# Performance work log

Measured on AMD Instinct MI355X. Metric: run time of the kernel, lower is better.

## Reference

```python
import jax, jax.numpy as jnp
import numpy as np

TAU = 1.0
NORMALIZE = True
EPS = 1e-16


def setup_inputs() -> dict:
    key = jax.random.key(0)
    k1, k2 = jax.random.split(key)
    N, D = 8192, 512
    xi = jax.random.normal(k1, (N, D), dtype=jnp.float32)
    xj = jax.random.normal(k2, (N, D), dtype=jnp.float32)
    return {"xi": xi, "xj": xj}


def reference(xi, xj):
    # sim_mat: [N, N] pairwise similarities
    sim_mat = xi @ xj.T
    if NORMALIZE:
        ni = jnp.linalg.norm(xi, axis=1)  # [N]
        nj = jnp.linalg.norm(xj, axis=1)  # [N]
        sim_mat = sim_mat / jnp.clip(ni[:, None] * nj[None, :], EPS)
    sim_mat = jnp.exp(sim_mat / TAU)
    # matched-pair similarity (diagonal-like term), [N]
    if NORMALIZE:
        sim_match = jnp.exp(jnp.sum(xi * xj, axis=-1) / (ni * nj) / TAU)
    else:
        sim_match = jnp.exp(jnp.sum(xi * xj, axis=-1) / TAU)
    sim_match = jnp.concatenate([sim_match, sim_match], axis=0)  # [2N]
    norm_sum = jnp.exp(jnp.ones((xi.shape[0],), dtype=xi.dtype) / TAU)  # [N]
    row_sum = jnp.sum(sim_mat, axis=-1) - norm_sum  # [N]
    # the torch source divides a [2N] vector by [N]; intended NT-Xent tiles the
    # denominator over both symmetric halves (values identical either way)
    row_sum = jnp.concatenate([row_sum, row_sum], axis=0)  # [2N]
    loss = jnp.mean(-jnp.log(sim_match / row_sum))
    return loss
```

## Files before the change

kernel.cpp:

```cpp
#include <hip/hip_runtime.h>
#include <stdint.h>

#define NR 8192
#define DIM 512
#define BT 128
#define BK 64
#define NT (DIM / BK)

typedef unsigned short u16;
typedef __attribute__((ext_vector_type(8))) __bf16 bf16x8;
typedef __attribute__((ext_vector_type(4))) float f32x4;

static __device__ __forceinline__ u16 f2bf(float f) {
    union { float f; uint32_t u; } v; v.f = f;
    uint32_t u = v.u;
    u += 0x7FFFu + ((u >> 16) & 1u);
    return (u16)(u >> 16);
}

static __device__ __forceinline__ void gload_lds16(const void* g, void* l) {
    __builtin_amdgcn_global_load_lds(
        (__attribute__((address_space(1))) void*)(void*)g,
        (__attribute__((address_space(3))) void*)l,
        16, 0, 0);
}

__global__ void prep_kernel(const float* __restrict__ xi, const float* __restrict__ xj,
                            u16* __restrict__ xib, u16* __restrict__ xjb,
                            float* __restrict__ inv_ni, float* __restrict__ inv_nj,
                            float* __restrict__ diag, float* __restrict__ rowsum) {
    const int row = blockIdx.x;
    const int t = threadIdx.x;
    const float4 a = ((const float4*)(xi + (size_t)row * DIM))[t];
    const float4 b = ((const float4*)(xj + (size_t)row * DIM))[t];

    float ssi = a.x*a.x + a.y*a.y + a.z*a.z + a.w*a.w;
    float ssj = b.x*b.x + b.y*b.y + b.z*b.z + b.w*b.w;
    float dot = a.x*b.x + a.y*b.y + a.z*b.z + a.w*b.w;

    ushort4 av = { f2bf(a.x), f2bf(a.y), f2bf(a.z), f2bf(a.w) };
    ushort4 bv = { f2bf(b.x), f2bf(b.y), f2bf(b.z), f2bf(b.w) };
    ((ushort4*)(xib + (size_t)row * DIM))[t] = av;
    ((ushort4*)(xjb + (size_t)row * DIM))[t] = bv;

    #pragma unroll
    for (int m = 32; m >= 1; m >>= 1) {
        ssi += __shfl_xor(ssi, m, 64);
        ssj += __shfl_xor(ssj, m, 64);
        dot += __shfl_xor(dot, m, 64);
    }
    __shared__ float red[6];
    const int wave = t >> 6, lane = t & 63;
    if (lane == 0) { red[wave*3+0] = ssi; red[wave*3+1] = ssj; red[wave*3+2] = dot; }
    __syncthreads();
    if (t == 0) {
        float si = red[0] + red[3];
        float sj = red[1] + red[4];
        float d  = red[2] + red[5];
        float ini = rsqrtf(fmaxf(si, 1e-30f));
        float inj = rsqrtf(fmaxf(sj, 1e-30f));
        inv_ni[row] = ini;
        inv_nj[row] = inj;
        diag[row] = d * ini * inj;
        rowsum[row] = 0.0f;
    }
}

__global__ __launch_bounds__(256, 4)
void gemm_rowsum(const u16* __restrict__ A, const u16* __restrict__ B,
                 const float* __restrict__ inv_ni, const float* __restrict__ inv_nj,
                 float* __restrict__ rowsum) {
    __shared__ __align__(16) u16 ldsA[BT * BK];
    __shared__ __align__(16) u16 ldsB[BT * BK];

    const int tid = threadIdx.x;
    const int orig = blockIdx.x;
    const int xcd = orig & 7, kidx = orig >> 3;
    const int by = xcd * 8 + (kidx & 7);
    const int bx = kidx >> 3;
    const int row0 = by * BT, col0 = bx * BT;

    const int st_row = tid >> 3;
    const int st_lc  = (tid & 7) ^ (st_row & 7);
    const u16* gA = A + (size_t)(row0 + st_row) * DIM + st_lc * 8;
    const u16* gB = B + (size_t)(col0 + st_row) * DIM + st_lc * 8;
    char* const dA = (char*)ldsA + tid * 16;
    char* const dB = (char*)ldsB + tid * 16;

    const int lane = tid & 63;
    const int lr = lane & 15, lk = lane >> 4;
    const int wid = tid >> 6;
    const int wm = wid >> 1, wn = wid & 1;
    const int sw = lr & 7;
    const int c0 = (lk ^ sw) * 16;
    const int c1 = ((4 + lk) ^ sw) * 16;
    const char* const aR = (const char*)ldsA + (wm * 64 + lr) * 128;
    const char* const bR = (const char*)ldsB + (wn * 64 + lr) * 128;

    f32x4 acc[4][4] = {};

    #pragma unroll 1
    for (int t = 0; t < NT; ++t) {
        if (t) __syncthreads();
        #pragma unroll
        for (int i = 0; i < 4; ++i) {
            gload_lds16(gA + t * BK + i * 32 * DIM, dA + i * 4096);
            gload_lds16(gB + t * BK + i * 32 * DIM, dB + i * 4096);
        }
        __syncthreads();

        #pragma unroll
        for (int kk = 0; kk < 2; ++kk) {
            const int cb = kk ? c1 : c0;
            bf16x8 af[4], bg[4];
            #pragma unroll
            for (int m = 0; m < 4; ++m)
                af[m] = *(const bf16x8*)(aR + m * 2048 + cb);
            #pragma unroll
            for (int n = 0; n < 4; ++n)
                bg[n] = *(const bf16x8*)(bR + n * 2048 + cb);
            #pragma unroll
            for (int m = 0; m < 4; ++m)
                #pragma unroll
                for (int n = 0; n < 4; ++n)
                    acc[m][n] = __builtin_amdgcn_mfma_f32_16x16x32_bf16(
                        af[m], bg[n], acc[m][n], 0, 0, 0);
        }
    }

    float inj[4];
    #pragma unroll
    for (int n = 0; n < 4; ++n)
        inj[n] = inv_nj[col0 + wn * 64 + n * 16 + lr];

    #pragma unroll
    for (int m = 0; m < 4; ++m) {
        #pragma unroll
        for (int e = 0; e < 4; ++e) {
            const int row = row0 + wm * 64 + m * 16 + lk * 4 + e;
            const float in_i = inv_ni[row];
            float s = 0.0f;
            #pragma unroll
            for (int n = 0; n < 4; ++n)
                s += __expf(acc[m][n][e] * in_i * inj[n]);
            s += __shfl_xor(s, 1, 64);
            s += __shfl_xor(s, 2, 64);
            s += __shfl_xor(s, 4, 64);
            s += __shfl_xor(s, 8, 64);
            if (lr == 0)
                atomicAdd(&rowsum[row], s);
        }
    }
}

__global__ void finalize(const float* __restrict__ rowsum,
                         const float* __restrict__ diag,
                         float* __restrict__ out) {
    const float E1 = 2.7182818284590452f;
    float acc = 0.0f;
    for (int i = threadIdx.x; i < NR; i += 256)
        acc += __logf(rowsum[i] - E1) - diag[i];
    #pragma unroll
    for (int m = 32; m >= 1; m >>= 1)
        acc += __shfl_xor(acc, m, 64);
    __shared__ float red[4];
    const int wave = threadIdx.x >> 6, lane = threadIdx.x & 63;
    if (lane == 0) red[wave] = acc;
    __syncthreads();
    if (threadIdx.x == 0)
        out[0] = (red[0] + red[1] + red[2] + red[3]) * (1.0f / NR);
}

extern "C" void kernel_launch(void* const* d_in, const int* in_sizes, int n_in,
                              void* d_out, int out_size, void* d_ws, size_t ws_size,
                              hipStream_t stream) {
    const float* xi = (const float*)d_in[0];
    const float* xj = (const float*)d_in[1];

    char* ws = (char*)d_ws;
    u16* xib = (u16*)ws;
    u16* xjb = xib + (size_t)NR * DIM;
    float* inv_ni = (float*)(xjb + (size_t)NR * DIM);
    float* inv_nj = inv_ni + NR;
    float* diag   = inv_nj + NR;
    float* rowsum = diag + NR;

    prep_kernel<<<NR, 128, 0, stream>>>(xi, xj, xib, xjb, inv_ni, inv_nj, diag, rowsum);
    gemm_rowsum<<<(NR / BT) * (NR / BT), 256, 0, stream>>>(xib, xjb, inv_ni, inv_nj, rowsum);
    finalize<<<1, 256, 0, stream>>>(rowsum, diag, (float*)d_out);
}
```

Measured before the change: 113.5 us.

## Rewrite GEMM as 256x256 tile with 32x32 MFMA and double-buffered LDS pipeline

Grows the block tile to 256x256 with 16 waves. It switches to 32x32x16 bf16 MFMA and double-buffers the LDS stages so global-to-LDS loads for the next K tile overlap compute. LDS reads use inline asm with explicit lgkmcnt waits, sched barriers and setprio to interleave ds_reads with MFMAs. The goal is better data reuse per loaded byte and hiding load latency. The cost is 128KB of LDS per block, which caps occupancy, and a more fragile hand-scheduled, fully unrolled K loop.

```diff
diff --git a/kernel.cpp b/kernel.cpp
--- a/kernel.cpp
+++ b/kernel.cpp
@@ -3,13 +3,13 @@
 
 #define NR 8192
 #define DIM 512
-#define BT 128
+#define BT 256
 #define BK 64
 #define NT (DIM / BK)
 
 typedef unsigned short u16;
 typedef __attribute__((ext_vector_type(8))) __bf16 bf16x8;
-typedef __attribute__((ext_vector_type(4))) float f32x4;
+typedef __attribute__((ext_vector_type(16))) float f32x16;
 
 static __device__ __forceinline__ u16 f2bf(float f) {
     union { float f; uint32_t u; } v; v.f = f;
@@ -23,6 +23,10 @@
         (__attribute__((address_space(1))) void*)(void*)g,
         (__attribute__((address_space(3))) void*)l,
         16, 0, 0);
+}
+
+static __device__ __forceinline__ uint32_t lds_addr(const void* p) {
+    return (uint32_t)(uintptr_t)(__attribute__((address_space(3))) const void*)p;
 }
 
 __global__ void prep_kernel(const float* __restrict__ xi, const float* __restrict__ xj,
@@ -66,88 +70,123 @@
     }
 }
 
-__global__ __launch_bounds__(256, 4)
+__global__ __launch_bounds__(1024, 4)
 void gemm_rowsum(const u16* __restrict__ A, const u16* __restrict__ B,
                  const float* __restrict__ inv_ni, const float* __restrict__ inv_nj,
                  float* __restrict__ rowsum) {
-    __shared__ __align__(16) u16 ldsA[BT * BK];
-    __shared__ __align__(16) u16 ldsB[BT * BK];
+    __shared__ __align__(16) u16 lds[4][16384];
 
     const int tid = threadIdx.x;
     const int orig = blockIdx.x;
     const int xcd = orig & 7, kidx = orig >> 3;
-    const int by = xcd * 8 + (kidx & 7);
-    const int bx = kidx >> 3;
+    const int by = xcd * 4 + (kidx & 3);
+    const int bx = kidx >> 2;
     const int row0 = by * BT, col0 = bx * BT;
 
     const int st_row = tid >> 3;
     const int st_lc  = (tid & 7) ^ (st_row & 7);
     const u16* gA = A + (size_t)(row0 + st_row) * DIM + st_lc * 8;
     const u16* gB = B + (size_t)(col0 + st_row) * DIM + st_lc * 8;
-    char* const dA = (char*)ldsA + tid * 16;
-    char* const dB = (char*)ldsB + tid * 16;
+    char* const ldsb = (char*)&lds[0][0];
+    char* const dsta = ldsb + tid * 16;
+    char* const dstb = ldsb + 65536 + tid * 16;
 
     const int lane = tid & 63;
-    const int lr = lane & 15, lk = lane >> 4;
+    const int l31 = lane & 31, hh = lane >> 5, sw = lane & 7;
     const int wid = tid >> 6;
-    const int wm = wid >> 1, wn = wid & 1;
-    const int sw = lr & 7;
-    const int c0 = (lk ^ sw) * 16;
-    const int c1 = ((4 + lk) ^ sw) * 16;
-    const char* const aR = (const char*)ldsA + (wm * 64 + lr) * 128;
-    const char* const bR = (const char*)ldsB + (wn * 64 + lr) * 128;
-
-    f32x4 acc[4][4] = {};
-
-    #pragma unroll 1
-    for (int t = 0; t < NT; ++t) {
-        if (t) __syncthreads();
+    const int wm = wid >> 2, wn = wid & 3;
+    const uint32_t ldsA32 = lds_addr(ldsb);
+    const uint32_t aoff = (wm * 64 + l31) * 128;
+    const uint32_t boff = (wn * 64 + l31) * 128;
+    const uint32_t cof0 = (uint32_t)(((0*2 + hh) ^ sw) * 16);
+    const uint32_t cof1 = (uint32_t)(((1*2 + hh) ^ sw) * 16);
+    const uint32_t cof2 = (uint32_t)(((2*2 + hh) ^ sw) * 16);
+    const uint32_t cof3 = (uint32_t)(((3*2 + hh) ^ sw) * 16);
+
+    f32x16 acc[2][2] = {};
+    bf16x8 af0[2], bg0[2], af1[2], bg1[2];
+
+#define DSR(D, ADDR) asm volatile("ds_read_b128 %0, %1" : "=v"(D) : "v"(ADDR))
+#define LGKM(N) asm volatile("s_waitcnt lgkmcnt(" #N ")" ::: "memory")
+#define SB0() __builtin_amdgcn_sched_barrier(0)
+#define BARR() __builtin_amdgcn_s_barrier()
+
+#define STAGE(P, TN) do {                                                      \
+    gload_lds16(gA + (TN) * BK,             dsta + (P) * 32768);               \
+    gload_lds16(gA + (TN) * BK + 128 * DIM, dsta + (P) * 32768 + 16384);       \
+    gload_lds16(gB + (TN) * BK,             dstb + (P) * 32768);               \
+    gload_lds16(gB + (TN) * BK + 128 * DIM, dstb + (P) * 32768 + 16384);       \
+} while (0)
+
+#define MM(AF, BG) do {                                                        \
+    __builtin_amdgcn_s_setprio(1);                                             \
+    acc[0][0] = __builtin_amdgcn_mfma_f32_32x32x16_bf16(AF[0], BG[0], acc[0][0], 0, 0, 0); \
+    acc[0][1] = __builtin_amdgcn_mfma_f32_32x32x16_bf16(AF[0], BG[1], acc[0][1], 0, 0, 0); \
+    acc[1][0] = __builtin_amdgcn_mfma_f32_32x32x16_bf16(AF[1], BG[0], acc[1][0], 0, 0, 0); \
+    acc[1][1] = __builtin_amdgcn_mfma_f32_32x32x16_bf16(AF[1], BG[1], acc[1][1], 0, 0, 0); \
+    __builtin_amdgcn_s_setprio(0);                                             \
+} while (0)
+
+#define TILE(P, ST, TN, VMSTR) do {                                            \
+    if (ST) STAGE((P) ^ 1, (TN) + 1);                                          \
+    asm volatile("s_waitcnt vmcnt(" VMSTR ")" ::: "memory");                   \
+    BARR();                                                                    \
+    const uint32_t ab = ldsA32 + (P) * 32768 + aoff;                           \
+    const uint32_t bb = ldsA32 + 65536 + (P) * 32768 + boff;                   \
+    DSR(af0[0], ab + cof0); DSR(af0[1], ab + 4096 + cof0);                     \
+    DSR(bg0[0], bb + cof0); DSR(bg0[1], bb + 4096 + cof0);                     \
+    DSR(af1[0], ab + cof1); DSR(af1[1], ab + 4096 + cof1);                     \
+    DSR(bg1[0], bb + cof1); DSR(bg1[1], bb + 4096 + cof1);                     \
+    LGKM(4); SB0();                                                            \
+    MM(af0, bg0);                                                     \
+    DSR(af0[0], ab + cof2); DSR(af0[1], ab + 4096 + cof2);                     \
+    DSR(bg0[0], bb + cof2); DSR(bg0[1], bb + 4096 + cof2);                     \
+    LGKM(4); SB0();                                                            \
+    MM(af1, bg1);                                                     \
+    DSR(af1[0], ab + cof3); DSR(af1[1], ab + 4096 + cof3);                     \
+    DSR(bg1[0], bb + cof3); DSR(bg1[1], bb + 4096 + cof3);                     \
+    LGKM(4); SB0();                                                            \
+    MM(af0, bg0);                                                     \
+    LGKM(0); SB0();                                                            \
+    BARR();                                       \
+    MM(af1, bg1);                                         \
+} while (0)
+
+    STAGE(0, 0);
+    TILE(0, 1, 0, "4");
+    TILE(1, 1, 1, "4");
+    TILE(0, 1, 2, "4");
+    TILE(1, 1, 3, "4");
+    TILE(0, 1, 4, "4");
+    TILE(1, 1, 5, "4");
+    TILE(0, 1, 6, "4");
+    TILE(1, 0, 7, "0");
+
+#undef DSR
+#undef LGKM
+#undef SB0
+#undef BARR
+#undef STAGE
+#undef MM
+#undef TILE
+
+    const float inj0 = inv_nj[col0 + wn * 64 + l31];
+    const float inj1 = inv_nj[col0 + wn * 64 + 32 + l31];
+
+    #pragma unroll
+    for (int mi = 0; mi < 2; ++mi) {
         #pragma unroll
-        for (int i = 0; i < 4; ++i) {
-            gload_lds16(gA + t * BK + i * 32 * DIM, dA + i * 4096);
-            gload_lds16(gB + t * BK + i * 32 * DIM, dB + i * 4096);
-        }
-        __syncthreads();
-
-        #pragma unroll
-        for (int kk = 0; kk < 2; ++kk) {
-            const int cb = kk ? c1 : c0;
-            bf16x8 af[4], bg[4];
-            #pragma unroll
-            for (int m = 0; m < 4; ++m)
-                af[m] = *(const bf16x8*)(aR + m * 2048 + cb);
-            #pragma unroll
-            for (int n = 0; n < 4; ++n)
-                bg[n] = *(const bf16x8*)(bR + n * 2048 + cb);
-            #pragma unroll
-            for (int m = 0; m < 4; ++m)
-                #pragma unroll
-                for (int n = 0; n < 4; ++n)
-                    acc[m][n] = __builtin_amdgcn_mfma_f32_16x16x32_bf16(
-                        af[m], bg[n], acc[m][n], 0, 0, 0);
-        }
-    }
-
-    float inj[4];
-    #pragma unroll
-    for (int n = 0; n < 4; ++n)
-        inj[n] = inv_nj[col0 + wn * 64 + n * 16 + lr];
-
-    #pragma unroll
-    for (int m = 0; m < 4; ++m) {
-        #pragma unroll
-        for (int e = 0; e < 4; ++e) {
-            const int row = row0 + wm * 64 + m * 16 + lk * 4 + e;
-            const float in_i = inv_ni[row];
-            float s = 0.0f;
-            #pragma unroll
-            for (int n = 0; n < 4; ++n)
-                s += __expf(acc[m][n][e] * in_i * inj[n]);
+        for (int r = 0; r < 16; ++r) {
+            const int row = row0 + wm * 64 + mi * 32 + (r & 3) + 8 * (r >> 2) + 4 * hh;
+            const float ini = inv_ni[row];
+            float s = __expf(acc[mi][0][r] * ini * inj0)
+                    + __expf(acc[mi][1][r] * ini * inj1);
             s += __shfl_xor(s, 1, 64);
             s += __shfl_xor(s, 2, 64);
             s += __shfl_xor(s, 4, 64);
             s += __shfl_xor(s, 8, 64);
-            if (lr == 0)
+            s += __shfl_xor(s, 16, 64);
+            if (l31 == 0)
                 atomicAdd(&rowsum[row], s);
         }
     }
@@ -186,6 +225,6 @@
     float* rowsum = diag + NR;
 
     prep_kernel<<<NR, 128, 0, stream>>>(xi, xj, xib, xjb, inv_ni, inv_nj, diag, rowsum);
-    gemm_rowsum<<<(NR / BT) * (NR / BT), 256, 0, stream>>>(xib, xjb, inv_ni, inv_nj, rowsum);
+    gemm_rowsum<<<(NR / BT) * (NR / BT), 1024, 0, stream>>>(xib, xjb, inv_ni, inv_nj, rowsum);
     finalize<<<1, 256, 0, stream>>>(rowsum, diag, (float*)d_out);
 }
```

Result: slower. 192.5 us (+69.6%).

## Double-buffer A tile in LDS and load B fragments directly from global

Applied to the files above, without the earlier changes.

Double-buffers the A tile in LDS so the load of the next K-step overlaps the MFMA work on the current one, with a single barrier per iteration. The B operand is no longer staged through LDS; each wave reads its B fragments straight from global memory into registers. This removes LDS traffic and one barrier for B but adds uncoalesced global loads per wave that depend on L2 hits, and it lowers the occupancy hint to 3 blocks per CU.

```diff
diff --git a/kernel.cpp b/kernel.cpp
--- a/kernel.cpp
+++ b/kernel.cpp
@@ -66,12 +66,11 @@
     }
 }
 
-__global__ __launch_bounds__(256, 4)
+__global__ __launch_bounds__(256, 3)
 void gemm_rowsum(const u16* __restrict__ A, const u16* __restrict__ B,
                  const float* __restrict__ inv_ni, const float* __restrict__ inv_nj,
                  float* __restrict__ rowsum) {
-    __shared__ __align__(16) u16 ldsA[BT * BK];
-    __shared__ __align__(16) u16 ldsB[BT * BK];
+    __shared__ __align__(16) u16 ldsA[2][BT * BK];
 
     const int tid = threadIdx.x;
     const int orig = blockIdx.x;
@@ -83,50 +82,69 @@
     const int st_row = tid >> 3;
     const int st_lc  = (tid & 7) ^ (st_row & 7);
     const u16* gA = A + (size_t)(row0 + st_row) * DIM + st_lc * 8;
-    const u16* gB = B + (size_t)(col0 + st_row) * DIM + st_lc * 8;
     char* const dA = (char*)ldsA + tid * 16;
-    char* const dB = (char*)ldsB + tid * 16;
 
     const int lane = tid & 63;
-    const int lr = lane & 15, lk = lane >> 4;
+    const int lr = lane & 15, lk = lane >> 4, sw = lr & 7;
     const int wid = tid >> 6;
     const int wm = wid >> 1, wn = wid & 1;
-    const int sw = lr & 7;
-    const int c0 = (lk ^ sw) * 16;
-    const int c1 = ((4 + lk) ^ sw) * 16;
-    const char* const aR = (const char*)ldsA + (wm * 64 + lr) * 128;
-    const char* const bR = (const char*)ldsB + (wn * 64 + lr) * 128;
+    const char* const aR0 = (const char*)ldsA + (wm * 64 + lr) * 128;
+    const int cb0 = (lk ^ sw) * 16;
+    const int cb1 = ((4 + lk) ^ sw) * 16;
+    const u16* const gB = B + (size_t)(col0 + wn * 64 + lr) * DIM + lk * 8;
 
     f32x4 acc[4][4] = {};
+
+#define STAGE(P, TN) do {                                                      \
+    _Pragma("unroll") for (int i = 0; i < 4; ++i)                              \
+        gload_lds16(gA + (TN) * BK + i * 32 * DIM, dA + (P) * 16384 + i * 4096); \
+} while (0)
+
+    STAGE(0, 0);
+    asm volatile("s_waitcnt vmcnt(0)" ::: "memory");
+    __builtin_amdgcn_s_barrier();
 
     #pragma unroll 1
     for (int t = 0; t < NT; ++t) {
-        if (t) __syncthreads();
-        #pragma unroll
-        for (int i = 0; i < 4; ++i) {
-            gload_lds16(gA + t * BK + i * 32 * DIM, dA + i * 4096);
-            gload_lds16(gB + t * BK + i * 32 * DIM, dB + i * 4096);
-        }
-        __syncthreads();
-
-        #pragma unroll
-        for (int kk = 0; kk < 2; ++kk) {
-            const int cb = kk ? c1 : c0;
-            bf16x8 af[4], bg[4];
-            #pragma unroll
-            for (int m = 0; m < 4; ++m)
-                af[m] = *(const bf16x8*)(aR + m * 2048 + cb);
+        const int p = t & 1;
+        if (t < NT - 1) STAGE(p ^ 1, t + 1);
+
+        const u16* gBt = gB + t * BK;
+        const char* aR = aR0 + p * 16384;
+
+        bf16x8 bg[4], af[4];
+        #pragma unroll
+        for (int n = 0; n < 4; ++n)
+            bg[n] = *(const bf16x8*)(gBt + n * 16 * DIM);
+        #pragma unroll
+        for (int m = 0; m < 4; ++m)
+            af[m] = *(const bf16x8*)(aR + m * 2048 + cb0);
+        #pragma unroll
+        for (int m = 0; m < 4; ++m)
             #pragma unroll
             for (int n = 0; n < 4; ++n)
-                bg[n] = *(const bf16x8*)(bR + n * 2048 + cb);
+                acc[m][n] = __builtin_amdgcn_mfma_f32_16x16x32_bf16(
+                    af[m], bg[n], acc[m][n], 0, 0, 0);
+
+        #pragma unroll
+        for (int n = 0; n < 4; ++n)
+            bg[n] = *(const bf16x8*)(gBt + n * 16 * DIM + 32);
+        #pragma unroll
+        for (int m = 0; m < 4; ++m)
+            af[m] = *(const bf16x8*)(aR + m * 2048 + cb1);
+        #pragma unroll
+        for (int m = 0; m < 4; ++m)
             #pragma unroll
-            for (int m = 0; m < 4; ++m)
-                #pragma unroll
-                for (int n = 0; n < 4; ++n)
-                    acc[m][n] = __builtin_amdgcn_mfma_f32_16x16x32_bf16(
-                        af[m], bg[n], acc[m][n], 0, 0, 0);
+            for (int n = 0; n < 4; ++n)
+                acc[m][n] = __builtin_amdgcn_mfma_f32_16x16x32_bf16(
+                    af[m], bg[n], acc[m][n], 0, 0, 0);
+
+        if (t < NT - 1) {
+            asm volatile("s_waitcnt vmcnt(0)" ::: "memory");
+            __builtin_amdgcn_s_barrier();
         }
     }
+#undef STAGE
 
     float inj[4];
     #pragma unroll
@@ -138,11 +156,11 @@
         #pragma unroll
         for (int e = 0; e < 4; ++e) {
             const int row = row0 + wm * 64 + m * 16 + lk * 4 + e;
-            const float in_i = inv_ni[row];
+            const float ini = inv_ni[row];
             float s = 0.0f;
             #pragma unroll
             for (int n = 0; n < 4; ++n)
-                s += __expf(acc[m][n][e] * in_i * inj[n]);
+                s += __expf(acc[m][n][e] * ini * inj[n]);
             s += __shfl_xor(s, 1, 64);
             s += __shfl_xor(s, 2, 64);
             s += __shfl_xor(s, 4, 64);
```

Measured after the change: 176.1 us. 1.55x slower.

## Double-buffer LDS tiles with BK=32 to overlap global loads with MFMA

Applied to the files above, without the earlier changes.

Halves the K tile to 32 and adds two LDS buffers, so the next tile's global-to-LDS loads are issued before computing on the current one. A single barrier per iteration replaces the two barriers around load and compute. The LDS swizzle is reworked for the 64-byte row stride. The trade-off is twice as many loop iterations and barriers, and only 16 MFMAs per barrier instead of 32.

```diff
diff --git a/kernel.cpp b/kernel.cpp
--- a/kernel.cpp
+++ b/kernel.cpp
@@ -4,7 +4,7 @@
 #define NR 8192
 #define DIM 512
 #define BT 128
-#define BK 64
+#define BK 32
 #define NT (DIM / BK)
 
 typedef unsigned short u16;
@@ -70,8 +70,8 @@
 void gemm_rowsum(const u16* __restrict__ A, const u16* __restrict__ B,
                  const float* __restrict__ inv_ni, const float* __restrict__ inv_nj,
                  float* __restrict__ rowsum) {
-    __shared__ __align__(16) u16 ldsA[BT * BK];
-    __shared__ __align__(16) u16 ldsB[BT * BK];
+    __shared__ __align__(16) u16 ldsA[2][BT * BK];
+    __shared__ __align__(16) u16 ldsB[2][BT * BK];
 
     const int tid = threadIdx.x;
     const int orig = blockIdx.x;
@@ -80,8 +80,8 @@
     const int bx = kidx >> 3;
     const int row0 = by * BT, col0 = bx * BT;
 
-    const int st_row = tid >> 3;
-    const int st_lc  = (tid & 7) ^ (st_row & 7);
+    const int st_row = tid >> 2;
+    const int st_lc  = (tid & 3) ^ ((st_row >> 1) & 3);
     const u16* gA = A + (size_t)(row0 + st_row) * DIM + st_lc * 8;
     const u16* gB = B + (size_t)(col0 + st_row) * DIM + st_lc * 8;
     char* const dA = (char*)ldsA + tid * 16;
@@ -89,44 +89,48 @@
 
     const int lane = tid & 63;
     const int lr = lane & 15, lk = lane >> 4;
+    const int cb = ((lk ^ ((lr >> 1) & 3))) * 16;
     const int wid = tid >> 6;
     const int wm = wid >> 1, wn = wid & 1;
-    const int sw = lr & 7;
-    const int c0 = (lk ^ sw) * 16;
-    const int c1 = ((4 + lk) ^ sw) * 16;
-    const char* const aR = (const char*)ldsA + (wm * 64 + lr) * 128;
-    const char* const bR = (const char*)ldsB + (wn * 64 + lr) * 128;
+    const char* const aR = (const char*)ldsA + (wm * 64 + lr) * 64 + cb;
+    const char* const bR = (const char*)ldsB + (wn * 64 + lr) * 64 + cb;
 
     f32x4 acc[4][4] = {};
 
+#define STAGE(P, TN) do {                                                      \
+    gload_lds16(gA + (TN) * BK,            dA + (P) * 8192);                   \
+    gload_lds16(gA + (TN) * BK + 64 * DIM, dA + (P) * 8192 + 4096);            \
+    gload_lds16(gB + (TN) * BK,            dB + (P) * 8192);                   \
+    gload_lds16(gB + (TN) * BK + 64 * DIM, dB + (P) * 8192 + 4096);            \
+} while (0)
+
+    STAGE(0, 0);
+    __syncthreads();
+
     #pragma unroll 1
     for (int t = 0; t < NT; ++t) {
-        if (t) __syncthreads();
+        const int p = t & 1;
+        if (t < NT - 1) STAGE(p ^ 1, t + 1);
+
+        const char* aP = aR + p * 8192;
+        const char* bP = bR + p * 8192;
+        bf16x8 af[4], bg[4];
         #pragma unroll
-        for (int i = 0; i < 4; ++i) {
-            gload_lds16(gA + t * BK + i * 32 * DIM, dA + i * 4096);
-            gload_lds16(gB + t * BK + i * 32 * DIM, dB + i * 4096);
-        }
-        __syncthreads();
-
+        for (int m = 0; m < 4; ++m)
+            af[m] = *(const bf16x8*)(aP + m * 1024);
         #pragma unroll
-        for (int kk = 0; kk < 2; ++kk) {
-            const int cb = kk ? c1 : c0;
-            bf16x8 af[4], bg[4];
-            #pragma unroll
-            for (int m = 0; m < 4; ++m)
-                af[m] = *(const bf16x8*)(aR + m * 2048 + cb);
+        for (int n = 0; n < 4; ++n)
+            bg[n] = *(const bf16x8*)(bP + n * 1024);
+        #pragma unroll
+        for (int m = 0; m < 4; ++m)
             #pragma unroll
             for (int n = 0; n < 4; ++n)
-                bg[n] = *(const bf16x8*)(bR + n * 2048 + cb);
-            #pragma unroll
-            for (int m = 0; m < 4; ++m)
-                #pragma unroll
-                for (int n = 0; n < 4; ++n)
-                    acc[m][n] = __builtin_amdgcn_mfma_f32_16x16x32_bf16(
-                        af[m], bg[n], acc[m][n], 0, 0, 0);
-        }
+                acc[m][n] = __builtin_amdgcn_mfma_f32_16x16x32_bf16(
+                    af[m], bg[n], acc[m][n], 0, 0, 0);
+
+        __syncthreads();
     }
+#undef STAGE
 
     float inj[4];
     #pragma unroll
@@ -138,11 +142,11 @@
         #pragma unroll
         for (int e = 0; e < 4; ++e) {
             const int row = row0 + wm * 64 + m * 16 + lk * 4 + e;
-            const float in_i = inv_ni[row];
+            const float ini = inv_ni[row];
             float s = 0.0f;
             #pragma unroll
             for (int n = 0; n < 4; ++n)
-                s += __expf(acc[m][n][e] * in_i * inj[n]);
+                s += __expf(acc[m][n][e] * ini * inj[n]);
             s += __shfl_xor(s, 1, 64);
             s += __shfl_xor(s, 2, 64);
             s += __shfl_xor(s, 4, 64);
```

Measured after the change: 128.5 us. +13.1%, slower.
